# Performance work log

Measured on AMD Instinct MI355X. Metric: run time of the kernel, lower is better.

## Reference

```python
import jax, jax.numpy as jnp
import numpy as np

NFFT = 1024
N_FREQ = NFFT // 2  # 512


def _ifft_kernels():
    # Intended kernels: exp(1j * 2*pi * t * f / nfft), columns 1..nfft/2,
    # scaled by 2 except the Nyquist column (last) which keeps weight 1.
    t = np.arange(NFFT, dtype=np.float64)[:, None]          # [1024, 1]
    f = np.arange(1, N_FREQ + 1, dtype=np.float64)[None, :]  # [1, 512]
    ang = 2.0 * np.pi * t * f / float(NFFT)
    real_k = 2.0 * np.cos(ang)
    imag_k = 2.0 * np.sin(ang)
    real_k[:, -1] /= 2.0
    imag_k[:, -1] /= 2.0
    return real_k.astype(np.float32), imag_k.astype(np.float32)


def setup_inputs() -> dict:
    key = jax.random.key(0)
    k1, k2 = jax.random.split(key)
    B, T = 8, 4096
    magn = jax.random.normal(k1, (B, 1, N_FREQ, T), dtype=jnp.float32)
    phase = jax.random.normal(k2, (B, 1, N_FREQ, T), dtype=jnp.float32)
    rk, ik = _ifft_kernels()
    return {
        "magn": magn,
        "phase": phase,
        "real_kernels": jnp.asarray(rk),   # [1024, 512]
        "imag_kernels": jnp.asarray(ik),   # [1024, 512]
    }


def reference(magn, phase, real_kernels, imag_kernels):
    # Conv2d(1, nfft, (n_freq, 1)) over [B,1,F,T] == dense matmul over freq axis.
    # out[b, c, t] = sum_f W[c, f] * x[b, f, t]
    m = magn[:, 0]   # [B, F, T]
    p = phase[:, 0]  # [B, F, T]
    out = jnp.einsum('cf,bft->bct', real_kernels, m) \
        - jnp.einsum('cf,bft->bct', imag_kernels, p)
    out = out[:, :, None, :] / NFFT  # [B, nfft, 1, T]
    return out
```

## Files before the change

kernel.cpp:

```cpp
#include <hip/hip_runtime.h>
#include <hip/hip_bf16.h>

#define NFREQ 512
#define KDIM  1024
#define CDIM  1024
#define TDIM  4096
#define BATCH 8
#define NT    16

typedef __bf16 bf16;
typedef __attribute__((ext_vector_type(8))) __bf16 bf16x8;
typedef __attribute__((ext_vector_type(4))) float f32x4;

__device__ __forceinline__ void gload_lds16(const bf16* g, void* l) {
    __builtin_amdgcn_global_load_lds(
        (const __attribute__((address_space(1))) void*)g,
        (__attribute__((address_space(3))) void*)l, 16, 0, 0);
}

__global__ __launch_bounds__(256) void prep_kc(const float* __restrict__ rk,
                                               const float* __restrict__ ik,
                                               bf16* __restrict__ Kc) {
    int idx = blockIdx.x * 256 + threadIdx.x;
    int c = idx >> 10;
    int k = idx & 1023;
    float v = (k < NFREQ) ? rk[c * NFREQ + k] : -ik[c * NFREQ + (k - NFREQ)];
    Kc[idx] = (bf16)(v * (1.0f / 1024.0f));
}

__global__ __launch_bounds__(256) void transpose_kernel(const float* __restrict__ magn,
                                                        const float* __restrict__ phase,
                                                        bf16* __restrict__ Xt) {
    __shared__ bf16 tile[64][68];
    const int tid = threadIdx.x;
    const int tt  = blockIdx.x & 63;
    const int ft  = blockIdx.x >> 6;
    const int b   = blockIdx.y;
    const int src = blockIdx.z;
    const float* in = src ? phase : magn;
    const int f0 = ft * 64, t0 = tt * 64;
    const size_t base = (size_t)b * NFREQ * TDIM;

    const int r0 = tid >> 4;
    const int c4 = (tid & 15) * 4;
#pragma unroll
    for (int i = 0; i < 4; i++) {
        int r = r0 + i * 16;
        const float4 v = *(const float4*)&in[base + (size_t)(f0 + r) * TDIM + t0 + c4];
        tile[r][c4 + 0] = (bf16)v.x;
        tile[r][c4 + 1] = (bf16)v.y;
        tile[r][c4 + 2] = (bf16)v.z;
        tile[r][c4 + 3] = (bf16)v.w;
    }
    __syncthreads();
    const int kbase = src * NFREQ + f0;
#pragma unroll
    for (int i = 0; i < 2; i++) {
        int ch = tid + 256 * i;
        int tr = ch >> 3;
        int c8 = (ch & 7) * 8;
        bf16x8 o;
#pragma unroll
        for (int j = 0; j < 8; j++) o[j] = tile[c8 + j][tr];
        *(bf16x8*)&Xt[((size_t)b * TDIM + t0 + tr) * KDIM + kbase + c8] = o;
    }
}

__global__ __launch_bounds__(512, 2) void gemm8(const bf16* __restrict__ Kc,
                                                const bf16* __restrict__ Xt,
                                                float* __restrict__ out) {
    extern __shared__ __align__(16) char smem[];

    const int tid = threadIdx.x;
    const int w = tid >> 6;
    const int l = tid & 63;

    const int x  = blockIdx.x;
    const int bm = x >> 4;
    const int bn = x & 15;
    const int b  = blockIdx.y;

    const bf16* Ab    = Kc + (size_t)(bm * 256) * KDIM;
    const bf16* Bbase = Xt + ((size_t)b * TDIM + bn * 256) * KDIM;

    const int srow   = ((w >> 2) * 128) + ((w & 3) * 8);
    const int ssub   = l >> 3;
    const int scol   = ((l & 7) ^ ssub) * 8;

    const int wr = w >> 2;
    const int wc = w & 3;
    const int fr = l & 15;
    const int l16 = l >> 4;
    const int fx = fr & 7;

    f32x4 acc[8][4] = {};

#define STAGE_A(curb, q, kt) \
    gload_lds16(Ab + (size_t)(srow + (q)*32 + ssub) * KDIM + (kt)*64 + scol, \
                smem + (curb)*65536 + (srow + (q)*32) * 128)
#define STAGE_B(curb, q, kt) \
    gload_lds16(Bbase + (size_t)(srow + (q)*32 + ssub) * KDIM + (kt)*64 + scol, \
                smem + (curb)*65536 + 32768 + (srow + (q)*32) * 128)

#pragma unroll
    for (int q = 0; q < 4; q++) STAGE_A(0, q, 0);
#pragma unroll
    for (int q = 0; q < 4; q++) STAGE_B(0, q, 0);
    STAGE_A(1, 0, 1); STAGE_A(1, 1, 1); STAGE_A(1, 2, 1);
    asm volatile("s_waitcnt vmcnt(3)" ::: "memory");
    __builtin_amdgcn_s_barrier();
    __builtin_amdgcn_sched_barrier(0);

    for (int v = 0; v < NT; ++v) {
        const int cur = v & 1;
        const char* At = smem + cur * 65536;
        const char* Bt = At + 32768;
        bf16x8 bfr[4][2];

#pragma unroll
        for (int p = 0; p < 4; p++) {
            bf16x8 afr[2][2];
#pragma unroll
            for (int mi = 0; mi < 2; mi++)
#pragma unroll
                for (int kk = 0; kk < 2; kk++) {
                    const int r = wr * 128 + (p * 2 + mi) * 16 + fr;
                    const int off = r * 128 + (((kk * 4 + l16) ^ fx) * 16);
                    afr[mi][kk] = *(const bf16x8*)(At + off);
                }
            if (p == 0) {
#pragma unroll
                for (int n = 0; n < 4; n++)
#pragma unroll
                    for (int kk = 0; kk < 2; kk++) {
                        const int r = wc * 64 + n * 16 + fr;
                        const int off = r * 128 + (((kk * 4 + l16) ^ fx) * 16);
                        bfr[n][kk] = *(const bf16x8*)(Bt + off);
                    }
            }

            if (p == 0) {
                if (v + 1 < NT) {
                    const int nc = cur ^ 1;
                    STAGE_A(nc, 3, v + 1);
                    STAGE_B(nc, 0, v + 1); STAGE_B(nc, 1, v + 1);
                    STAGE_B(nc, 2, v + 1); STAGE_B(nc, 3, v + 1);
                }
            } else {
                if (v + 2 < NT) STAGE_A(cur, p - 1, v + 2);
            }

            __builtin_amdgcn_s_barrier();
            __builtin_amdgcn_s_setprio(1);
#pragma unroll
            for (int mi = 0; mi < 2; mi++)
#pragma unroll
                for (int n = 0; n < 4; n++)
#pragma unroll
                    for (int kk = 0; kk < 2; kk++)
                        acc[p * 2 + mi][n] = __builtin_amdgcn_mfma_f32_16x16x32_bf16(
                            afr[mi][kk], bfr[n][kk], acc[p * 2 + mi][n], 0, 0, 0);
            __builtin_amdgcn_s_setprio(0);
            if (p == 3) {
                if (v < NT - 2) { asm volatile("s_waitcnt vmcnt(3)" ::: "memory"); }
                else            { asm volatile("s_waitcnt vmcnt(0)" ::: "memory"); }
            }
            __builtin_amdgcn_s_barrier();
            __builtin_amdgcn_sched_barrier(0);
        }
    }
#undef STAGE_A
#undef STAGE_B

    const int cr = l16 * 4;
    const int cc = fr;
    float* obase = out + ((size_t)b * CDIM + bm * 256 + wr * 128) * TDIM + bn * 256 + wc * 64;
#pragma unroll
    for (int m = 0; m < 8; m++)
#pragma unroll
        for (int n = 0; n < 4; n++)
#pragma unroll
            for (int j = 0; j < 4; j++)
                obase[(size_t)(m * 16 + cr + j) * TDIM + n * 16 + cc] = acc[m][n][j];
}

__global__ __launch_bounds__(256) void naive_kernel(const float* __restrict__ m,
                                                    const float* __restrict__ p,
                                                    const float* __restrict__ rk,
                                                    const float* __restrict__ ik,
                                                    float* __restrict__ out) {
    size_t idx = (size_t)blockIdx.x * 256 + threadIdx.x;
    int t = idx & 4095;
    size_t r = idx >> 12;
    int c = (int)(r & 1023);
    int b = (int)(r >> 10);
    float acc = 0.f;
    for (int f = 0; f < NFREQ; f++) {
        acc += rk[c * NFREQ + f] * m[((size_t)b * NFREQ + f) * TDIM + t]
             - ik[c * NFREQ + f] * p[((size_t)b * NFREQ + f) * TDIM + t];
    }
    out[idx] = acc * (1.0f / 1024.0f);
}

extern "C" void kernel_launch(void* const* d_in, const int* in_sizes, int n_in,
                              void* d_out, int out_size, void* d_ws, size_t ws_size,
                              hipStream_t stream) {
    const float* magn  = (const float*)d_in[0];
    const float* phase = (const float*)d_in[1];
    const float* rk    = (const float*)d_in[2];
    const float* ik    = (const float*)d_in[3];
    float* out = (float*)d_out;

    const size_t kc_bytes = (size_t)CDIM * KDIM * sizeof(bf16);
    const size_t xt_bytes = (size_t)BATCH * TDIM * KDIM * sizeof(bf16);
    if (ws_size < kc_bytes + xt_bytes) {
        naive_kernel<<<(CDIM * TDIM * BATCH) / 256, 256, 0, stream>>>(magn, phase, rk, ik, out);
        return;
    }

    bf16* Kc = (bf16*)d_ws;
    bf16* Xt = (bf16*)((char*)d_ws + kc_bytes);

    (void)hipFuncSetAttribute((const void*)gemm8,
                              hipFuncAttributeMaxDynamicSharedMemorySize, 131072);

    prep_kc<<<(CDIM * KDIM) / 256, 256, 0, stream>>>(rk, ik, Kc);
    transpose_kernel<<<dim3(512, BATCH, 2), 256, 0, stream>>>(magn, phase, Xt);
    gemm8<<<dim3(64, BATCH), 512, 131072, stream>>>(Kc, Xt, out);
}
```

Measured before the change: 121.6 us.

## Fuse fp32-to-bf16 transpose of magn/phase into GEMM B-tile loading

After: 148.8 us. 1.22x slower.

```diff
diff --git a/kernel.cpp b/kernel.cpp
--- a/kernel.cpp
+++ b/kernel.cpp
@@ -28,46 +28,9 @@
     Kc[idx] = (bf16)(v * (1.0f / 1024.0f));
 }
 
-__global__ __launch_bounds__(256) void transpose_kernel(const float* __restrict__ magn,
-                                                        const float* __restrict__ phase,
-                                                        bf16* __restrict__ Xt) {
-    __shared__ bf16 tile[64][68];
-    const int tid = threadIdx.x;
-    const int tt  = blockIdx.x & 63;
-    const int ft  = blockIdx.x >> 6;
-    const int b   = blockIdx.y;
-    const int src = blockIdx.z;
-    const float* in = src ? phase : magn;
-    const int f0 = ft * 64, t0 = tt * 64;
-    const size_t base = (size_t)b * NFREQ * TDIM;
-
-    const int r0 = tid >> 4;
-    const int c4 = (tid & 15) * 4;
-#pragma unroll
-    for (int i = 0; i < 4; i++) {
-        int r = r0 + i * 16;
-        const float4 v = *(const float4*)&in[base + (size_t)(f0 + r) * TDIM + t0 + c4];
-        tile[r][c4 + 0] = (bf16)v.x;
-        tile[r][c4 + 1] = (bf16)v.y;
-        tile[r][c4 + 2] = (bf16)v.z;
-        tile[r][c4 + 3] = (bf16)v.w;
-    }
-    __syncthreads();
-    const int kbase = src * NFREQ + f0;
-#pragma unroll
-    for (int i = 0; i < 2; i++) {
-        int ch = tid + 256 * i;
-        int tr = ch >> 3;
-        int c8 = (ch & 7) * 8;
-        bf16x8 o;
-#pragma unroll
-        for (int j = 0; j < 8; j++) o[j] = tile[c8 + j][tr];
-        *(bf16x8*)&Xt[((size_t)b * TDIM + t0 + tr) * KDIM + kbase + c8] = o;
-    }
-}
-
-__global__ __launch_bounds__(512, 2) void gemm8(const bf16* __restrict__ Kc,
-                                                const bf16* __restrict__ Xt,
+__global__ __launch_bounds__(512, 2) void gemmf(const bf16* __restrict__ Kc,
+                                                const float* __restrict__ magn,
+                                                const float* __restrict__ phase,
                                                 float* __restrict__ out) {
     extern __shared__ __align__(16) char smem[];
 
@@ -80,34 +43,47 @@
     const int bn = x & 15;
     const int b  = blockIdx.y;
 
-    const bf16* Ab    = Kc + (size_t)(bm * 256) * KDIM;
-    const bf16* Bbase = Xt + ((size_t)b * TDIM + bn * 256) * KDIM;
-
-    const int srow   = ((w >> 2) * 128) + ((w & 3) * 8);
-    const int ssub   = l >> 3;
-    const int scol   = ((l & 7) ^ ssub) * 8;
+    const bf16* Ab = Kc + (size_t)(bm * 256) * KDIM;
+
+    const int srow = ((w >> 2) * 128) + ((w & 3) * 8);
+    const int ssub = l >> 3;
 
     const int wr = w >> 2;
     const int wc = w & 3;
     const int fr = l & 15;
     const int l16 = l >> 4;
-    const int fx = fr & 7;
+
+    const float* mb = magn + (size_t)b * NFREQ * TDIM + (size_t)(8 * w) * TDIM + bn * 256 + 4 * l;
+    const float* pb = phase + (size_t)b * NFREQ * TDIM + (size_t)(8 * w) * TDIM + bn * 256 + 4 * l;
 
     f32x4 acc[8][4] = {};
+    float4 bld[8];
 
 #define STAGE_A(curb, q, kt) \
-    gload_lds16(Ab + (size_t)(srow + (q)*32 + ssub) * KDIM + (kt)*64 + scol, \
+    gload_lds16(Ab + (size_t)(srow + (q)*32 + ssub) * KDIM + (kt)*64 \
+                   + (((l & 7) ^ ssub ^ (w & 3) ^ ((((q)&1)) << 2)) * 8), \
                 smem + (curb)*65536 + (srow + (q)*32) * 128)
-#define STAGE_B(curb, q, kt) \
-    gload_lds16(Bbase + (size_t)(srow + (q)*32 + ssub) * KDIM + (kt)*64 + scol, \
-                smem + (curb)*65536 + 32768 + (srow + (q)*32) * 128)
-
-#pragma unroll
-    for (int q = 0; q < 4; q++) STAGE_A(0, q, 0);
-#pragma unroll
-    for (int q = 0; q < 4; q++) STAGE_B(0, q, 0);
-    STAGE_A(1, 0, 1); STAGE_A(1, 1, 1); STAGE_A(1, 2, 1);
-    asm volatile("s_waitcnt vmcnt(3)" ::: "memory");
+
+#define BLOAD(vn) { \
+    const float* s_ = (((vn) < 8) ? mb : pb) + (size_t)(((vn) & 7) * 64) * TDIM; \
+    _Pragma("unroll") \
+    for (int j = 0; j < 8; j++) bld[j] = *(const float4*)(s_ + (size_t)j * TDIM); }
+
+#define BWRITE(dstB) { \
+    _Pragma("unroll") \
+    for (int c = 0; c < 4; c++) { \
+        bf16x8 o_; \
+        _Pragma("unroll") \
+        for (int j = 0; j < 8; j++) o_[j] = (bf16)(((const float*)&bld[j])[c]); \
+        const int t_ = 4 * l + c; \
+        const int sw_ = (t_ & 7) ^ ((l >> 1) & 7); \
+        *(bf16x8*)((dstB) + t_ * 128 + ((w ^ sw_) * 16)) = o_; } }
+
+    BLOAD(0);
+    STAGE_A(0, 0, 0); STAGE_A(0, 1, 0); STAGE_A(0, 2, 0); STAGE_A(0, 3, 0);
+    BWRITE(smem + 32768);
+    asm volatile("s_waitcnt vmcnt(0)" ::: "memory");
+    asm volatile("s_waitcnt lgkmcnt(0)" ::: "memory");
     __builtin_amdgcn_s_barrier();
     __builtin_amdgcn_sched_barrier(0);
 
@@ -115,62 +91,65 @@
         const int cur = v & 1;
         const char* At = smem + cur * 65536;
         const char* Bt = At + 32768;
-        bf16x8 bfr[4][2];
+        char* Bn = smem + (cur ^ 1) * 65536 + 32768;
+        const bool more = (v + 1 < NT);
+        bf16x8 ah[8];
 
 #pragma unroll
         for (int p = 0; p < 4; p++) {
-            bf16x8 afr[2][2];
-#pragma unroll
-            for (int mi = 0; mi < 2; mi++)
-#pragma unroll
-                for (int kk = 0; kk < 2; kk++) {
-                    const int r = wr * 128 + (p * 2 + mi) * 16 + fr;
-                    const int off = r * 128 + (((kk * 4 + l16) ^ fx) * 16);
-                    afr[mi][kk] = *(const bf16x8*)(At + off);
-                }
-            if (p == 0) {
-#pragma unroll
-                for (int n = 0; n < 4; n++)
+            const int ph = p >> 1;
+            const int pn = p & 1;
+
+            if (pn == 0) {
+#pragma unroll
+                for (int mi = 0; mi < 4; mi++)
 #pragma unroll
                     for (int kk = 0; kk < 2; kk++) {
-                        const int r = wc * 64 + n * 16 + fr;
-                        const int off = r * 128 + (((kk * 4 + l16) ^ fx) * 16);
-                        bfr[n][kk] = *(const bf16x8*)(Bt + off);
+                        const int M = ph * 4 + mi;
+                        const int r = wr * 128 + M * 16 + fr;
+                        const int fx = (fr & 7) ^ ((M * 2 + (fr >> 3)) & 7);
+                        ah[mi * 2 + kk] = *(const bf16x8*)(At + r * 128 + (((kk * 4 + l16) ^ fx) * 16));
                     }
             }
-
-            if (p == 0) {
-                if (v + 1 < NT) {
-                    const int nc = cur ^ 1;
-                    STAGE_A(nc, 3, v + 1);
-                    STAGE_B(nc, 0, v + 1); STAGE_B(nc, 1, v + 1);
-                    STAGE_B(nc, 2, v + 1); STAGE_B(nc, 3, v + 1);
+            bf16x8 bh[2][2];
+#pragma unroll
+            for (int ni = 0; ni < 2; ni++)
+#pragma unroll
+                for (int kk = 0; kk < 2; kk++) {
+                    const int n = pn * 2 + ni;
+                    const int r = wc * 64 + n * 16 + fr;
+                    const int fx = (fr & 7) ^ ((n * 2 + (fr >> 3)) & 7);
+                    bh[ni][kk] = *(const bf16x8*)(Bt + r * 128 + (((kk * 4 + l16) ^ fx) * 16));
                 }
-            } else {
-                if (v + 2 < NT) STAGE_A(cur, p - 1, v + 2);
-            }
+
+            if (p == 0)      { if (more) BLOAD(v + 1); }
+            else if (p == 1) { if (more) { STAGE_A(cur ^ 1, 0, v + 1); STAGE_A(cur ^ 1, 1, v + 1); } }
+            else if (p == 2) { if (more) { STAGE_A(cur ^ 1, 2, v + 1); STAGE_A(cur ^ 1, 3, v + 1); } }
 
             __builtin_amdgcn_s_barrier();
             __builtin_amdgcn_s_setprio(1);
 #pragma unroll
-            for (int mi = 0; mi < 2; mi++)
-#pragma unroll
-                for (int n = 0; n < 4; n++)
+            for (int mi = 0; mi < 4; mi++)
+#pragma unroll
+                for (int ni = 0; ni < 2; ni++)
 #pragma unroll
                     for (int kk = 0; kk < 2; kk++)
-                        acc[p * 2 + mi][n] = __builtin_amdgcn_mfma_f32_16x16x32_bf16(
-                            afr[mi][kk], bfr[n][kk], acc[p * 2 + mi][n], 0, 0, 0);
+                        acc[ph * 4 + mi][pn * 2 + ni] = __builtin_amdgcn_mfma_f32_16x16x32_bf16(
+                            ah[mi * 2 + kk], bh[ni][kk], acc[ph * 4 + mi][pn * 2 + ni], 0, 0, 0);
             __builtin_amdgcn_s_setprio(0);
+
             if (p == 3) {
-                if (v < NT - 2) { asm volatile("s_waitcnt vmcnt(3)" ::: "memory"); }
-                else            { asm volatile("s_waitcnt vmcnt(0)" ::: "memory"); }
+                if (more) BWRITE(Bn);
+                asm volatile("s_waitcnt vmcnt(0)" ::: "memory");
+                asm volatile("s_waitcnt lgkmcnt(0)" ::: "memory");
             }
             __builtin_amdgcn_s_barrier();
             __builtin_amdgcn_sched_barrier(0);
         }
     }
 #undef STAGE_A
-#undef STAGE_B
+#undef BLOAD
+#undef BWRITE
 
     const int cr = l16 * 4;
     const int cc = fr;
@@ -212,19 +191,16 @@
     float* out = (float*)d_out;
 
     const size_t kc_bytes = (size_t)CDIM * KDIM * sizeof(bf16);
-    const size_t xt_bytes = (size_t)BATCH * TDIM * KDIM * sizeof(bf16);
-    if (ws_size < kc_bytes + xt_bytes) {
+    if (ws_size < kc_bytes) {
         naive_kernel<<<(CDIM * TDIM * BATCH) / 256, 256, 0, stream>>>(magn, phase, rk, ik, out);
         return;
     }
 
     bf16* Kc = (bf16*)d_ws;
-    bf16* Xt = (bf16*)((char*)d_ws + kc_bytes);
-
-    (void)hipFuncSetAttribute((const void*)gemm8,
+
+    (void)hipFuncSetAttribute((const void*)gemmf,
                               hipFuncAttributeMaxDynamicSharedMemorySize, 131072);
 
     prep_kc<<<(CDIM * KDIM) / 256, 256, 0, stream>>>(rk, ik, Kc);
-    transpose_kernel<<<dim3(512, BATCH, 2), 256, 0, stream>>>(magn, phase, Xt);
-    gemm8<<<dim3(64, BATCH), 512, 131072, stream>>>(Kc, Xt, out);
-}
+    gemmf<<<dim3(64, BATCH), 512, 131072, stream>>>(Kc, magn, phase, out);
+}
```
